# Performance work log

Measured on AMD Instinct MI355X. Metric: run time of the kernel, lower is better.

## Reference

```python
import jax, jax.numpy as jnp
import numpy as np

N = 50000
E = 800000
B = 64
NODE_IN, EDGE_IN, H, OUT_DIM = 16, 8, 64, 2


def _glorot(key, shape):
    fan_in, fan_out = shape[0], shape[-1]
    s = jnp.sqrt(6.0 / (fan_in + fan_out))
    return jax.random.uniform(key, shape, jnp.float32, -s, s)


def setup_inputs() -> dict:
    key = jax.random.key(0)
    ks = jax.random.split(key, 32)
    inp = {
        'x': jax.random.normal(ks[0], (N, NODE_IN), jnp.float32),
        'edge_index': jax.random.randint(ks[1], (2, E), 0, N).astype(jnp.int64),
        'edge_attr': jax.random.normal(ks[2], (E, EDGE_IN), jnp.float32),
        'batch': jnp.sort(jax.random.randint(ks[3], (N,), 0, B)).astype(jnp.int64),
        # encoders
        'W_node': _glorot(ks[4], (NODE_IN, H)), 'b_node': jnp.zeros((H,), jnp.float32),
        'W_edge': _glorot(ks[5], (EDGE_IN, H)), 'b_edge': jnp.zeros((H,), jnp.float32),
        # conv1: GATv2, heads=4, concat=True, edge_dim=H
        'Wl1': _glorot(ks[6], (H, 4 * H)), 'bl1': jnp.zeros((4 * H,), jnp.float32),
        'Wr1': _glorot(ks[7], (H, 4 * H)), 'br1': jnp.zeros((4 * H,), jnp.float32),
        'We1': _glorot(ks[8], (H, 4 * H)),
        'att1': _glorot(ks[9], (4, H)),
        'bias1': jnp.zeros((4 * H,), jnp.float32),
        # conv2: GATv2, heads=1, concat=False, in=4H
        'Wl2': _glorot(ks[10], (4 * H, H)), 'bl2': jnp.zeros((H,), jnp.float32),
        'Wr2': _glorot(ks[11], (4 * H, H)), 'br2': jnp.zeros((H,), jnp.float32),
        'We2': _glorot(ks[12], (H, H)),
        'att2': _glorot(ks[13], (1, H)),
        'bias2': jnp.zeros((H,), jnp.float32),
        # decoder
        'Wd1': _glorot(ks[14], (H, H)), 'bd1': jnp.zeros((H,), jnp.float32),
        'Wd2': _glorot(ks[15], (H, OUT_DIM)), 'bd2': jnp.zeros((OUT_DIM,), jnp.float32),
    }
    return inp


def _gatv2(x, src, dst, eattr, Wl, bl, Wr, br, We, att, bias, heads, out_ch, concat):
    n = x.shape[0]
    # add self-loops with edge_attr fill_value='mean' (segment mean over dst), PyG default
    ones = jnp.ones((src.shape[0],), x.dtype)
    deg = jax.ops.segment_sum(ones, dst, num_segments=n)
    loop_attr = jax.ops.segment_sum(eattr, dst, num_segments=n) / jnp.clip(deg, 1.0)[:, None]
    ea = jnp.concatenate([eattr, loop_attr], 0)               # [E+N, F_e]
    s = jnp.concatenate([src, jnp.arange(n)], 0)
    d = jnp.concatenate([dst, jnp.arange(n)], 0)
    xl = (x @ Wl + bl).reshape(n, heads, out_ch)              # source transform
    xr = (x @ Wr + br).reshape(n, heads, out_ch)              # target transform
    ep = (ea @ We).reshape(-1, heads, out_ch)                 # edge transform (no bias)
    m = jax.nn.leaky_relu(xl[s] + xr[d] + ep, 0.2)            # [E+N, heads, out_ch]
    logits = jnp.einsum('ehc,hc->eh', m, att)
    lmax = jax.ops.segment_max(logits, d, num_segments=n)
    lmax = jnp.where(jnp.isfinite(lmax), lmax, 0.0)
    a = jnp.exp(logits - lmax[d])
    denom = jax.ops.segment_sum(a, d, num_segments=n)
    alpha = a / (denom[d] + 1e-16)                            # segment softmax over dst
    out = jax.ops.segment_sum(alpha[..., None] * xl[s], d, num_segments=n)
    out = out.reshape(n, heads * out_ch) if concat else out.mean(1)
    return out + bias


def reference(x, edge_index, edge_attr, batch, W_node, b_node, W_edge, b_edge,
              Wl1, bl1, Wr1, br1, We1, att1, bias1,
              Wl2, bl2, Wr2, br2, We2, att2, bias2,
              Wd1, bd1, Wd2, bd2):
    src, dst = edge_index[0], edge_index[1]
    h = x @ W_node + b_node
    ea = edge_attr @ W_edge + b_edge
    h = jax.nn.elu(_gatv2(h, src, dst, ea, Wl1, bl1, Wr1, br1, We1, att1, bias1, 4, H, True))
    h = _gatv2(h, src, dst, ea, Wl2, bl2, Wr2, br2, We2, att2, bias2, 1, H, False)
    # global mean pool over batch vector
    cnt = jax.ops.segment_sum(jnp.ones((h.shape[0],), h.dtype), batch, num_segments=B)
    pooled = jax.ops.segment_sum(h, batch, num_segments=B) / jnp.clip(cnt, 1.0)[:, None]
    out = jax.nn.relu(pooled @ Wd1 + bd1) @ Wd2 + bd2
    return jax.nn.sigmoid(out)
```

## Files before the change

kernel.cpp:

```cpp
#include <hip/hip_runtime.h>
#include <math.h>

#define NN 50000
#define NE 800000
#define NB 64

__device__ __forceinline__ int permpos(int c) {
  return ((c & 63) << 2) | (((c >> 6) ^ c) & 3);
}

__global__ void k_zero(int* __restrict__ p, int n) {
  int i = blockIdx.x * blockDim.x + threadIdx.x;
  if (i < n) p[i] = 0;
}

__global__ void k_fuse(const float* __restrict__ Wn, const float* __restrict__ bn,
                       const float* __restrict__ We, const float* __restrict__ be,
                       const float* __restrict__ Wl1, const float* __restrict__ bl1,
                       const float* __restrict__ Wr1, const float* __restrict__ br1,
                       const float* __restrict__ We1, const float* __restrict__ We2,
                       const float* __restrict__ att1, const float* __restrict__ bias1,
                       float* __restrict__ wl1e, float* __restrict__ bl1e,
                       float* __restrict__ wr1e, float* __restrict__ br1e,
                       float* __restrict__ wfe1, float* __restrict__ bfe1,
                       float* __restrict__ wfe2, float* __restrict__ bfe2,
                       float* __restrict__ att1p, float* __restrict__ bias1p) {
  int t = blockIdx.x * blockDim.x + threadIdx.x;
  if (t < 4096) {
    int i = t >> 8, j = t & 255; float s = 0.f;
    for (int k = 0; k < 64; k++) s += Wn[i * 64 + k] * Wl1[k * 256 + j];
    wl1e[i * 256 + permpos(j)] = s;
  } else if (t < 8192) {
    int u = t - 4096; int i = u >> 8, j = u & 255; float s = 0.f;
    for (int k = 0; k < 64; k++) s += Wn[i * 64 + k] * Wr1[k * 256 + j];
    wr1e[i * 256 + permpos(j)] = s;
  } else if (t < 10240) {
    int u = t - 8192; int i = u >> 8, j = u & 255; float s = 0.f;
    for (int k = 0; k < 64; k++) s += We[i * 64 + k] * We1[k * 256 + j];
    wfe1[i * 256 + permpos(j)] = s;
  } else if (t < 10752) {
    int u = t - 10240; int i = u >> 6, j = u & 63; float s = 0.f;
    for (int k = 0; k < 64; k++) s += We[i * 64 + k] * We2[k * 64 + j];
    wfe2[u] = s;
  } else if (t < 11008) {
    int j = t - 10752; float s = bl1[j];
    for (int k = 0; k < 64; k++) s += bn[k] * Wl1[k * 256 + j];
    bl1e[permpos(j)] = s;
  } else if (t < 11264) {
    int j = t - 11008; float s = br1[j];
    for (int k = 0; k < 64; k++) s += bn[k] * Wr1[k * 256 + j];
    br1e[permpos(j)] = s;
  } else if (t < 11520) {
    int j = t - 11264; float s = 0.f;
    for (int k = 0; k < 64; k++) s += be[k] * We1[k * 256 + j];
    bfe1[permpos(j)] = s;
  } else if (t < 11584) {
    int j = t - 11520; float s = 0.f;
    for (int k = 0; k < 64; k++) s += be[k] * We2[k * 64 + j];
    bfe2[j] = s;
  } else if (t < 11840) {
    int j = t - 11584;
    att1p[permpos(j)] = att1[j];
  } else if (t < 12096) {
    int j = t - 11840;
    bias1p[permpos(j)] = bias1[j];
  }
}

__global__ void k_deg(const int* __restrict__ dstA, int* __restrict__ deg) {
  int e = blockIdx.x * blockDim.x + threadIdx.x;
  if (e < NE) atomicAdd(&deg[dstA[e]], 1);
}

__global__ __launch_bounds__(1024) void k_scan1(const int* __restrict__ deg,
                                                int* __restrict__ incl, int* __restrict__ partials) {
  __shared__ int sm[1024];
  int i = blockIdx.x * 1024 + threadIdx.x;
  int v = (i < NN) ? (deg[i] + 1) : 0;
  sm[threadIdx.x] = v;
  __syncthreads();
  for (int off = 1; off < 1024; off <<= 1) {
    int t = (threadIdx.x >= off) ? sm[threadIdx.x - off] : 0;
    __syncthreads();
    sm[threadIdx.x] += t;
    __syncthreads();
  }
  if (i < NN) incl[i] = sm[threadIdx.x];
  if (threadIdx.x == 1023) partials[blockIdx.x] = sm[1023];
}

__global__ void k_scan2(int* __restrict__ partials, int* __restrict__ rowptr, int nblk) {
  int t = threadIdx.x;
  int v = (t < nblk) ? partials[t] : 0;
  for (int off = 1; off < 64; off <<= 1) {
    int u = __shfl_up(v, off, 64);
    if (t >= off) v += u;
  }
  if (t < nblk) partials[t] = v;
  if (t == nblk - 1) rowptr[NN] = v;
}

__global__ void k_scan3(const int* __restrict__ deg, const int* __restrict__ incl,
                        const int* __restrict__ partials, int* __restrict__ rowptr) {
  int i = blockIdx.x * blockDim.x + threadIdx.x;
  if (i >= NN) return;
  int blk = i >> 10;
  int base = blk ? partials[blk - 1] : 0;
  rowptr[i] = base + incl[i] - (deg[i] + 1);
}

__global__ void k_csr(const int* __restrict__ srcA, const int* __restrict__ dstA,
                      const int* __restrict__ rowptr, const int* __restrict__ deg,
                      int* __restrict__ cursor, int2* __restrict__ csr) {
  int t = blockIdx.x * blockDim.x + threadIdx.x;
  if (t < NE) {
    int d = dstA[t];
    int pos = rowptr[d] + atomicAdd(&cursor[d], 1);
    csr[pos] = make_int2(t, srcA[t]);
  } else if (t < NE + NN) {
    int n = t - NE;
    csr[rowptr[n] + deg[n]] = make_int2(NE + n, n);
  }
}

__global__ __launch_bounds__(256) void k_loop8(const int* __restrict__ rowptr,
                                               const int2* __restrict__ csr,
                                               const float* __restrict__ eattr,
                                               float* __restrict__ lattr) {
  int d = (blockIdx.x * blockDim.x + threadIdx.x) >> 6;
  int lane = threadIdx.x & 63;
  if (d >= NN) return;
  int beg = rowptr[d], endReal = rowptr[d + 1] - 1;
  int k = lane & 7, sub = lane >> 3;
  float s = 0.f;
  for (int i = beg + sub; i < endReal; i += 8) {
    int eid = csr[i].x;
    s += eattr[(size_t)eid * 8 + k];
  }
  s += __shfl_xor(s, 8, 64);
  s += __shfl_xor(s, 16, 64);
  s += __shfl_xor(s, 32, 64);
  float invdeg = 1.f / fmaxf((float)(endReal - beg), 1.f);
  if (lane < 8) lattr[(size_t)d * 8 + lane] = s * invdeg;
}

__global__ __launch_bounds__(256) void k_lin1(const float* __restrict__ x,
                                              const float* __restrict__ wl, const float* __restrict__ bl,
                                              const float* __restrict__ wr, const float* __restrict__ br,
                                              float* __restrict__ xl, float* __restrict__ xr) {
  __shared__ float xs[4][16];
  int nb = blockIdx.x * 4;
  int t = threadIdx.x;
  if (t < 64) xs[t >> 4][t & 15] = x[nb * 16 + t];
  __syncthreads();
  float accl[4], accr[4];
  float blv = bl[t], brv = br[t];
#pragma unroll
  for (int u = 0; u < 4; u++) { accl[u] = blv; accr[u] = brv; }
#pragma unroll
  for (int k = 0; k < 16; k++) {
    float wlv = wl[k * 256 + t], wrv = wr[k * 256 + t];
#pragma unroll
    for (int u = 0; u < 4; u++) {
      accl[u] += xs[u][k] * wlv;
      accr[u] += xs[u][k] * wrv;
    }
  }
#pragma unroll
  for (int u = 0; u < 4; u++) {
    xl[(size_t)(nb + u) * 256 + t] = accl[u];
    xr[(size_t)(nb + u) * 256 + t] = accr[u];
  }
}

__device__ __forceinline__ void load_ek(const float* __restrict__ eattr,
                                        const float* __restrict__ lattr,
                                        int eid, float ek[8]) {
  const float* b; int ei;
  if (eid < NE) { b = eattr; ei = eid; } else { b = lattr; ei = eid - NE; }
  const float* p = b + (size_t)ei * 8;
#pragma unroll
  for (int k = 0; k < 8; k++) ek[k] = p[k];
}

__device__ __forceinline__ float jreduce(float part[4]) {
  part[0] += __shfl_xor(part[1], 1, 64);
  part[2] += __shfl_xor(part[3], 1, 64);
  float v = part[0] + __shfl_xor(part[2], 2, 64);
  v += __shfl_xor(v, 4, 64);
  v += __shfl_xor(v, 8, 64);
  v += __shfl_xor(v, 16, 64);
  v += __shfl_xor(v, 32, 64);
  return v;
}

__global__ __launch_bounds__(256) void k_conv1(
    const float* __restrict__ eattr, const float* __restrict__ lattr,
    const int* __restrict__ rowptr, const int2* __restrict__ csr,
    const float* __restrict__ xl, const float* __restrict__ xrg,
    const float* __restrict__ att1p, const float* __restrict__ bias1p,
    const float* __restrict__ wfe1, const float* __restrict__ bfe1,
    float* __restrict__ out1) {
  int d = __builtin_amdgcn_readfirstlane((blockIdx.x * blockDim.x + threadIdx.x) >> 6);
  int lane = threadIdx.x & 63;
  if (d >= NN) return;
  int l4 = lane << 2;
  float4 xr4 = *(const float4*)(xrg + (size_t)d * 256 + l4);
  float4 at4 = *(const float4*)(att1p + l4);
  float4 bf4 = *(const float4*)(bfe1 + l4);
  float4 wf[8];
#pragma unroll
  for (int k = 0; k < 8; k++) wf[k] = *(const float4*)(wfe1 + k * 256 + l4);

  float acc0 = 0.f, acc1 = 0.f, acc2 = 0.f, acc3 = 0.f;
  float mrun = -INFINITY, lrun = 0.f;
  int beg = rowptr[d], end = rowptr[d + 1];

  auto epart = [&](int eid, const float4& x4, float part[4]) {
    float ek[8];
    load_ek(eattr, lattr, eid, ek);
    float e0 = bf4.x, e1 = bf4.y, e2 = bf4.z, e3 = bf4.w;
#pragma unroll
    for (int k = 0; k < 8; k++) {
      e0 += ek[k] * wf[k].x;
      e1 += ek[k] * wf[k].y;
      e2 += ek[k] * wf[k].z;
      e3 += ek[k] * wf[k].w;
    }
    float m0 = x4.x + xr4.x + e0; m0 = (m0 > 0.f) ? m0 : 0.2f * m0;
    float m1 = x4.y + xr4.y + e1; m1 = (m1 > 0.f) ? m1 : 0.2f * m1;
    float m2 = x4.z + xr4.z + e2; m2 = (m2 > 0.f) ? m2 : 0.2f * m2;
    float m3 = x4.w + xr4.w + e3; m3 = (m3 > 0.f) ? m3 : 0.2f * m3;
    part[0] = at4.x * m0; part[1] = at4.y * m1;
    part[2] = at4.z * m2; part[3] = at4.w * m3;
  };

  int idx = beg;
  for (; idx + 4 <= end; idx += 4) {
    int2 e0 = csr[idx], e1 = csr[idx + 1], e2 = csr[idx + 2], e3 = csr[idx + 3];
    float4 x0 = *(const float4*)(xl + (size_t)e0.y * 256 + l4);
    float4 x1 = *(const float4*)(xl + (size_t)e1.y * 256 + l4);
    float4 x2 = *(const float4*)(xl + (size_t)e2.y * 256 + l4);
    float4 x3 = *(const float4*)(xl + (size_t)e3.y * 256 + l4);
    float pa[4], pb[4], pc[4], pd[4];
    epart(e0.x, x0, pa); epart(e1.x, x1, pb);
    epart(e2.x, x2, pc); epart(e3.x, x3, pd);
    float v0 = jreduce(pa), v1 = jreduce(pb), v2 = jreduce(pc), v3 = jreduce(pd);
    float gmax = fmaxf(fmaxf(v0, v1), fmaxf(v2, v3));
    if (__ballot(gmax > mrun)) {
      float nm = fmaxf(mrun, gmax);
      float sc = __expf(mrun - nm);
      mrun = nm; lrun *= sc;
      float sc1 = __shfl_xor(sc, 1, 64);
      float sc2 = __shfl_xor(sc, 2, 64);
      float sc3 = __shfl_xor(sc1, 2, 64);
      acc0 *= sc; acc1 *= sc1; acc2 *= sc2; acc3 *= sc3;
    }
    float q0 = __expf(v0 - mrun), q1 = __expf(v1 - mrun);
    float q2 = __expf(v2 - mrun), q3 = __expf(v3 - mrun);
    lrun += q0 + q1 + q2 + q3;
    {
      float a1 = __shfl_xor(q0, 1, 64), a2 = __shfl_xor(q0, 2, 64), a3 = __shfl_xor(a1, 2, 64);
      acc0 += q0 * x0.x; acc1 += a1 * x0.y; acc2 += a2 * x0.z; acc3 += a3 * x0.w;
    }
    {
      float a1 = __shfl_xor(q1, 1, 64), a2 = __shfl_xor(q1, 2, 64), a3 = __shfl_xor(a1, 2, 64);
      acc0 += q1 * x1.x; acc1 += a1 * x1.y; acc2 += a2 * x1.z; acc3 += a3 * x1.w;
    }
    {
      float a1 = __shfl_xor(q2, 1, 64), a2 = __shfl_xor(q2, 2, 64), a3 = __shfl_xor(a1, 2, 64);
      acc0 += q2 * x2.x; acc1 += a1 * x2.y; acc2 += a2 * x2.z; acc3 += a3 * x2.w;
    }
    {
      float a1 = __shfl_xor(q3, 1, 64), a2 = __shfl_xor(q3, 2, 64), a3 = __shfl_xor(a1, 2, 64);
      acc0 += q3 * x3.x; acc1 += a1 * x3.y; acc2 += a2 * x3.z; acc3 += a3 * x3.w;
    }
  }
  for (; idx < end; ++idx) {
    int2 e0 = csr[idx];
    float4 x0 = *(const float4*)(xl + (size_t)e0.y * 256 + l4);
    float pa[4];
    epart(e0.x, x0, pa);
    float v0 = jreduce(pa);
    if (__ballot(v0 > mrun)) {
      float nm = fmaxf(mrun, v0);
      float sc = __expf(mrun - nm);
      mrun = nm; lrun *= sc;
      float sc1 = __shfl_xor(sc, 1, 64);
      float sc2 = __shfl_xor(sc, 2, 64);
      float sc3 = __shfl_xor(sc1, 2, 64);
      acc0 *= sc; acc1 *= sc1; acc2 *= sc2; acc3 *= sc3;
    }
    float q0 = __expf(v0 - mrun);
    lrun += q0;
    float a1 = __shfl_xor(q0, 1, 64), a2 = __shfl_xor(q0, 2, 64), a3 = __shfl_xor(a1, 2, 64);
    acc0 += q0 * x0.x; acc1 += a1 * x0.y; acc2 += a2 * x0.z; acc3 += a3 * x0.w;
  }

  float lr0 = lrun;
  float lr1 = __shfl_xor(lr0, 1, 64);
  float lr2 = __shfl_xor(lr0, 2, 64);
  float lr3 = __shfl_xor(lr1, 2, 64);
  float4 bi4 = *(const float4*)(bias1p + l4);
  float4 o;
  o.x = acc0 / (lr0 + 1e-16f) + bi4.x;
  o.y = acc1 / (lr1 + 1e-16f) + bi4.y;
  o.z = acc2 / (lr2 + 1e-16f) + bi4.z;
  o.w = acc3 / (lr3 + 1e-16f) + bi4.w;
  o.x = (o.x > 0.f) ? o.x : (__expf(o.x) - 1.f);
  o.y = (o.y > 0.f) ? o.y : (__expf(o.y) - 1.f);
  o.z = (o.z > 0.f) ? o.z : (__expf(o.z) - 1.f);
  o.w = (o.w > 0.f) ? o.w : (__expf(o.w) - 1.f);
  *(float4*)(out1 + (size_t)d * 256 + l4) = o;
}

__global__ __launch_bounds__(256) void k_lin2(const float* __restrict__ in,
                                              const float* __restrict__ wl, const float* __restrict__ bl,
                                              const float* __restrict__ wr, const float* __restrict__ br,
                                              float* __restrict__ xl, float* __restrict__ xr) {
  int col = threadIdx.x & 63;
  int grp = threadIdx.x >> 6;
  int node0 = blockIdx.x * 16 + grp * 4;
  float sl[4], sr[4];
  float blv = bl[col], brv = br[col];
#pragma unroll
  for (int u = 0; u < 4; u++) { sl[u] = blv; sr[u] = brv; }
  const float4* r0 = (const float4*)(in + (size_t)(node0 + 0) * 256);
  const float4* r1 = (const float4*)(in + (size_t)(node0 + 1) * 256);
  const float4* r2 = (const float4*)(in + (size_t)(node0 + 2) * 256);
  const float4* r3 = (const float4*)(in + (size_t)(node0 + 3) * 256);
#pragma unroll 4
  for (int g4 = 0; g4 < 64; g4++) {
    int b = g4 & 3;
    int i0 = ((0 ^ b) << 6) + g4;
    int i1 = ((1 ^ b) << 6) + g4;
    int i2 = ((2 ^ b) << 6) + g4;
    int i3 = ((3 ^ b) << 6) + g4;
    float wl0 = wl[i0 * 64 + col], wl1v = wl[i1 * 64 + col];
    float wl2v = wl[i2 * 64 + col], wl3v = wl[i3 * 64 + col];
    float wr0 = wr[i0 * 64 + col], wr1v = wr[i1 * 64 + col];
    float wr2v = wr[i2 * 64 + col], wr3v = wr[i3 * 64 + col];
    float4 v0 = r0[g4], v1 = r1[g4], v2 = r2[g4], v3 = r3[g4];
    sl[0] += v0.x * wl0 + v0.y * wl1v + v0.z * wl2v + v0.w * wl3v;
    sl[1] += v1.x * wl0 + v1.y * wl1v + v1.z * wl2v + v1.w * wl3v;
    sl[2] += v2.x * wl0 + v2.y * wl1v + v2.z * wl2v + v2.w * wl3v;
    sl[3] += v3.x * wl0 + v3.y * wl1v + v3.z * wl2v + v3.w * wl3v;
    sr[0] += v0.x * wr0 + v0.y * wr1v + v0.z * wr2v + v0.w * wr3v;
    sr[1] += v1.x * wr0 + v1.y * wr1v + v1.z * wr2v + v1.w * wr3v;
    sr[2] += v2.x * wr0 + v2.y * wr1v + v2.z * wr2v + v2.w * wr3v;
    sr[3] += v3.x * wr0 + v3.y * wr1v + v3.z * wr2v + v3.w * wr3v;
  }
#pragma unroll
  for (int u = 0; u < 4; u++) {
    xl[(size_t)(node0 + u) * 64 + col] = sl[u];
    xr[(size_t)(node0 + u) * 64 + col] = sr[u];
  }
}

__global__ __launch_bounds__(256) void k_conv2(
    const float* __restrict__ eattr, const float* __restrict__ lattr,
    const int* __restrict__ rowptr, const int2* __restrict__ csr,
    const float* __restrict__ xl, const float* __restrict__ xrg,
    const float* __restrict__ att2, const float* __restrict__ bias2,
    const float* __restrict__ wfe2, const float* __restrict__ bfe2,
    float* __restrict__ out2) {
  int d = __builtin_amdgcn_readfirstlane((blockIdx.x * blockDim.x + threadIdx.x) >> 6);
  int lane = threadIdx.x & 63;
  if (d >= NN) return;
  float xr_l = xrg[(size_t)d * 64 + lane];
  float att_l = att2[lane];
  float bfe_l = bfe2[lane];
  float wfe_l[8];
#pragma unroll
  for (int k = 0; k < 8; k++) wfe_l[k] = wfe2[k * 64 + lane];
  float acc = 0.f, mrun = -INFINITY, lrun = 0.f;
  int beg = rowptr[d], end = rowptr[d + 1];

  auto elogit = [&](int eid, float xs) {
    float ek[8];
    load_ek(eattr, lattr, eid, ek);
    float ep = bfe_l;
#pragma unroll
    for (int k = 0; k < 8; k++) ep += ek[k] * wfe_l[k];
    float m = xs + xr_l + ep;
    m = (m > 0.f) ? m : 0.2f * m;
    float v = att_l * m;
    v += __shfl_xor(v, 1, 64);
    v += __shfl_xor(v, 2, 64);
    v += __shfl_xor(v, 4, 64);
    v += __shfl_xor(v, 8, 64);
    v += __shfl_xor(v, 16, 64);
    v += __shfl_xor(v, 32, 64);
    return v;
  };

  int idx = beg;
  for (; idx + 4 <= end; idx += 4) {
    int2 e0 = csr[idx], e1 = csr[idx + 1], e2 = csr[idx + 2], e3 = csr[idx + 3];
    float x0 = xl[(size_t)e0.y * 64 + lane];
    float x1 = xl[(size_t)e1.y * 64 + lane];
    float x2 = xl[(size_t)e2.y * 64 + lane];
    float x3 = xl[(size_t)e3.y * 64 + lane];
    float v0 = elogit(e0.x, x0), v1 = elogit(e1.x, x1);
    float v2 = elogit(e2.x, x2), v3 = elogit(e3.x, x3);
    float gmax = fmaxf(fmaxf(v0, v1), fmaxf(v2, v3));
    if (gmax > mrun) {
      float sc = __expf(mrun - gmax);
      mrun = gmax; lrun *= sc; acc *= sc;
    }
    float q0 = __expf(v0 - mrun), q1 = __expf(v1 - mrun);
    float q2 = __expf(v2 - mrun), q3 = __expf(v3 - mrun);
    lrun += q0 + q1 + q2 + q3;
    acc += q0 * x0 + q1 * x1 + q2 * x2 + q3 * x3;
  }
  for (; idx < end; ++idx) {
    int2 e0 = csr[idx];
    float x0 = xl[(size_t)e0.y * 64 + lane];
    float v0 = elogit(e0.x, x0);
    if (v0 > mrun) {
      float sc = __expf(mrun - v0);
      mrun = v0; lrun *= sc; acc *= sc;
    }
    float q0 = __expf(v0 - mrun);
    lrun += q0;
    acc += q0 * x0;
  }
  out2[(size_t)d * 64 + lane] = acc / (lrun + 1e-16f) + bias2[lane];
}

__device__ __forceinline__ int lowerb(const int* a, int n, int v) {
  int lo = 0, hi = n;
  while (lo < hi) {
    int mid = (lo + hi) >> 1;
    if (a[mid] < v) lo = mid + 1; else hi = mid;
  }
  return lo;
}

__global__ __launch_bounds__(256) void k_pool(const int* __restrict__ batch,
                                              const float* __restrict__ out2,
                                              float* __restrict__ pooled) {
  int b = blockIdx.x;
  int start = lowerb(batch, NN, b);
  int end = lowerb(batch, NN, b + 1);
  int c = threadIdx.x & 63, sub = threadIdx.x >> 6;
  float s = 0.f;
  for (int i = start + sub; i < end; i += 4) s += out2[(size_t)i * 64 + c];
  __shared__ float sm[256];
  sm[threadIdx.x] = s;
  __syncthreads();
  if (sub == 0) {
    float tot = sm[c] + sm[64 + c] + sm[128 + c] + sm[192 + c];
    float cnt = fmaxf((float)(end - start), 1.f);
    pooled[b * 64 + c] = tot / cnt;
  }
}

__global__ __launch_bounds__(1024) void k_dec(const float* __restrict__ pooled,
                                              const float* __restrict__ Wd1, const float* __restrict__ bd1,
                                              const float* __restrict__ Wd2, const float* __restrict__ bd2,
                                              float* __restrict__ out) {
  __shared__ float hid[64 * 64];
  int t = threadIdx.x;
  for (int i = t; i < 4096; i += 1024) {
    int b = i >> 6, j = i & 63;
    float s = bd1[j];
#pragma unroll 8
    for (int k = 0; k < 64; k++) s += pooled[b * 64 + k] * Wd1[k * 64 + j];
    hid[i] = fmaxf(s, 0.f);
  }
  __syncthreads();
  if (t < 128) {
    int b = t >> 1, o = t & 1;
    float s = bd2[o];
#pragma unroll 8
    for (int k = 0; k < 64; k++) s += hid[b * 64 + k] * Wd2[k * 2 + o];
    out[t] = 1.f / (1.f + __expf(-s));
  }
}

extern "C" void kernel_launch(void* const* d_in, const int* in_sizes, int n_in,
                              void* d_out, int out_size, void* d_ws, size_t ws_size,
                              hipStream_t stream) {
  const float* x     = (const float*)d_in[0];
  const int*   eidx  = (const int*)d_in[1];
  const float* eattr = (const float*)d_in[2];
  const int*   batch = (const int*)d_in[3];
  const float* Wn    = (const float*)d_in[4];
  const float* bn    = (const float*)d_in[5];
  const float* We    = (const float*)d_in[6];
  const float* be    = (const float*)d_in[7];
  const float* Wl1   = (const float*)d_in[8];
  const float* bl1   = (const float*)d_in[9];
  const float* Wr1   = (const float*)d_in[10];
  const float* br1   = (const float*)d_in[11];
  const float* We1   = (const float*)d_in[12];
  const float* att1  = (const float*)d_in[13];
  const float* bias1 = (const float*)d_in[14];
  const float* Wl2   = (const float*)d_in[15];
  const float* bl2   = (const float*)d_in[16];
  const float* Wr2   = (const float*)d_in[17];
  const float* br2   = (const float*)d_in[18];
  const float* We2   = (const float*)d_in[19];
  const float* att2  = (const float*)d_in[20];
  const float* bias2 = (const float*)d_in[21];
  const float* Wd1   = (const float*)d_in[22];
  const float* bd1   = (const float*)d_in[23];
  const float* Wd2   = (const float*)d_in[24];
  const float* bd2   = (const float*)d_in[25];

  const int* srcA = eidx;
  const int* dstA = eidx + NE;

  char* ws = (char*)d_ws;
  size_t off = 0;
  auto alloc = [&](size_t bytes) -> char* {
    char* p = ws + off;
    off += (bytes + 255) & ~(size_t)255;
    return p;
  };

  int*   deg    = (int*)alloc(NN * 4);
  int*   cursor = (int*)alloc(NN * 4);
  size_t zero_bytes = off;
  int*   rowptr   = (int*)alloc((NN + 1) * 4);
  int*   incl     = (int*)alloc(NN * 4);
  int*   partials = (int*)alloc(64 * 4);
  int2*  csr      = (int2*)alloc((size_t)(NE + NN + 1) * 8);
  float* lattr = (float*)alloc((size_t)NN * 8 * 4);
  float* wl1e  = (float*)alloc(4096 * 4);
  float* wr1e  = (float*)alloc(4096 * 4);
  float* wfe1  = (float*)alloc(2048 * 4);
  float* wfe2  = (float*)alloc(512 * 4);
  float* bl1e  = (float*)alloc(256 * 4);
  float* br1e  = (float*)alloc(256 * 4);
  float* bfe1  = (float*)alloc(256 * 4);
  float* bfe2  = (float*)alloc(64 * 4);
  float* att1p = (float*)alloc(256 * 4);
  float* bias1p= (float*)alloc(256 * 4);
  float* xl1   = (float*)alloc((size_t)NN * 256 * 4);
  float* xr1   = (float*)alloc((size_t)NN * 256 * 4);
  float* out1  = (float*)alloc((size_t)NN * 256 * 4);
  float* xl2   = (float*)alloc((size_t)NN * 64 * 4);
  float* xr2   = (float*)alloc((size_t)NN * 64 * 4);
  float* out2  = (float*)alloc((size_t)NN * 64 * 4);
  float* pooled = (float*)alloc((size_t)NB * 64 * 4);

  int zn = (int)(zero_bytes / 4);
  int nscan = (NN + 1023) / 1024;
  k_zero<<<(zn + 255) / 256, 256, 0, stream>>>((int*)d_ws, zn);
  k_fuse<<<(12096 + 255) / 256, 256, 0, stream>>>(Wn, bn, We, be, Wl1, bl1, Wr1, br1, We1, We2,
                                                  att1, bias1,
                                                  wl1e, bl1e, wr1e, br1e, wfe1, bfe1, wfe2, bfe2,
                                                  att1p, bias1p);
  k_deg<<<(NE + 255) / 256, 256, 0, stream>>>(dstA, deg);
  k_scan1<<<nscan, 1024, 0, stream>>>(deg, incl, partials);
  k_scan2<<<1, 64, 0, stream>>>(partials, rowptr, nscan);
  k_scan3<<<(NN + 255) / 256, 256, 0, stream>>>(deg, incl, partials, rowptr);
  k_csr<<<(NE + NN + 255) / 256, 256, 0, stream>>>(srcA, dstA, rowptr, deg, cursor, csr);
  k_loop8<<<(NN + 3) / 4, 256, 0, stream>>>(rowptr, csr, eattr, lattr);
  k_lin1<<<NN / 4, 256, 0, stream>>>(x, wl1e, bl1e, wr1e, br1e, xl1, xr1);
  k_conv1<<<(NN + 3) / 4, 256, 0, stream>>>(eattr, lattr, rowptr, csr, xl1, xr1,
                                            att1p, bias1p, wfe1, bfe1, out1);
  k_lin2<<<NN / 16, 256, 0, stream>>>(out1, Wl2, bl2, Wr2, br2, xl2, xr2);
  k_conv2<<<(NN + 3) / 4, 256, 0, stream>>>(eattr, lattr, rowptr, csr, xl2, xr2,
                                            att2, bias2, wfe2, bfe2, out2);
  k_pool<<<NB, 256, 0, stream>>>(batch, out2, pooled);
  k_dec<<<1, 1024, 0, stream>>>(pooled, Wd1, bd1, Wd2, bd2, (float*)d_out);
}
```

Measured before the change: 771.4 us.

## Store gathered source features as bf16 and restructure conv/lin reductions

```diff
diff --git a/kernel.cpp b/kernel.cpp
--- a/kernel.cpp
+++ b/kernel.cpp
@@ -7,6 +7,15 @@
 
 __device__ __forceinline__ int permpos(int c) {
   return ((c & 63) << 2) | (((c >> 6) ^ c) & 3);
+}
+
+__device__ __forceinline__ unsigned short f2bf(float f) {
+  unsigned int u = __float_as_uint(f);
+  u += 0x7fffu + ((u >> 16) & 1u);
+  return (unsigned short)(u >> 16);
+}
+__device__ __forceinline__ float bf2f(unsigned short b) {
+  return __uint_as_float(((unsigned int)b) << 16);
 }
 
 __global__ void k_zero(int* __restrict__ p, int n) {
@@ -147,40 +156,34 @@
 __global__ __launch_bounds__(256) void k_lin1(const float* __restrict__ x,
                                               const float* __restrict__ wl, const float* __restrict__ bl,
                                               const float* __restrict__ wr, const float* __restrict__ br,
-                                              float* __restrict__ xl, float* __restrict__ xr) {
+                                              unsigned short* __restrict__ xl, float* __restrict__ xr) {
   __shared__ float xs[4][16];
   int nb = blockIdx.x * 4;
   int t = threadIdx.x;
   if (t < 64) xs[t >> 4][t & 15] = x[nb * 16 + t];
   __syncthreads();
-  float accl[4], accr[4];
-  float blv = bl[t], brv = br[t];
-#pragma unroll
-  for (int u = 0; u < 4; u++) { accl[u] = blv; accr[u] = brv; }
+  int w = t >> 6, lane = t & 63, l4 = lane << 2;
+  float4 accl = *(const float4*)(bl + l4);
+  float4 accr = *(const float4*)(br + l4);
+  const float* xrow = xs[w];
 #pragma unroll
   for (int k = 0; k < 16; k++) {
-    float wlv = wl[k * 256 + t], wrv = wr[k * 256 + t];
-#pragma unroll
-    for (int u = 0; u < 4; u++) {
-      accl[u] += xs[u][k] * wlv;
-      accr[u] += xs[u][k] * wrv;
-    }
-  }
-#pragma unroll
-  for (int u = 0; u < 4; u++) {
-    xl[(size_t)(nb + u) * 256 + t] = accl[u];
-    xr[(size_t)(nb + u) * 256 + t] = accr[u];
-  }
-}
-
-__device__ __forceinline__ void load_ek(const float* __restrict__ eattr,
-                                        const float* __restrict__ lattr,
-                                        int eid, float ek[8]) {
-  const float* b; int ei;
-  if (eid < NE) { b = eattr; ei = eid; } else { b = lattr; ei = eid - NE; }
-  const float* p = b + (size_t)ei * 8;
-#pragma unroll
-  for (int k = 0; k < 8; k++) ek[k] = p[k];
+    float xv = xrow[k];
+    float4 wl4 = *(const float4*)(wl + k * 256 + l4);
+    float4 wr4 = *(const float4*)(wr + k * 256 + l4);
+    accl.x += xv * wl4.x; accl.y += xv * wl4.y; accl.z += xv * wl4.z; accl.w += xv * wl4.w;
+    accr.x += xv * wr4.x; accr.y += xv * wr4.y; accr.z += xv * wr4.z; accr.w += xv * wr4.w;
+  }
+  int node = nb + w;
+  ushort4 us;
+  us.x = f2bf(accl.x); us.y = f2bf(accl.y); us.z = f2bf(accl.z); us.w = f2bf(accl.w);
+  *(ushort4*)(xl + (size_t)node * 256 + l4) = us;
+  *(float4*)(xr + (size_t)node * 256 + l4) = accr;
+}
+
+__device__ __forceinline__ const float* ek_ptr(const float* __restrict__ eattr,
+                                               const float* __restrict__ lattr, int eid) {
+  return (eid < NE) ? (eattr + (size_t)eid * 8) : (lattr + (size_t)(eid - NE) * 8);
 }
 
 __device__ __forceinline__ float jreduce(float part[4]) {
@@ -197,7 +200,7 @@
 __global__ __launch_bounds__(256) void k_conv1(
     const float* __restrict__ eattr, const float* __restrict__ lattr,
     const int* __restrict__ rowptr, const int2* __restrict__ csr,
-    const float* __restrict__ xl, const float* __restrict__ xrg,
+    const unsigned short* __restrict__ xl, const float* __restrict__ xrg,
     const float* __restrict__ att1p, const float* __restrict__ bias1p,
     const float* __restrict__ wfe1, const float* __restrict__ bfe1,
     float* __restrict__ out1) {
@@ -216,16 +219,18 @@
   float mrun = -INFINITY, lrun = 0.f;
   int beg = rowptr[d], end = rowptr[d + 1];
 
-  auto epart = [&](int eid, const float4& x4, float part[4]) {
-    float ek[8];
-    load_ek(eattr, lattr, eid, ek);
+  auto ld4 = [&](int s) -> float4 {
+    ushort4 u = *(const ushort4*)(xl + (size_t)s * 256 + l4);
+    float4 f; f.x = bf2f(u.x); f.y = bf2f(u.y); f.z = bf2f(u.z); f.w = bf2f(u.w);
+    return f;
+  };
+  auto epart = [&](const float* __restrict__ p, const float4& x4, float part[4]) {
     float e0 = bf4.x, e1 = bf4.y, e2 = bf4.z, e3 = bf4.w;
 #pragma unroll
     for (int k = 0; k < 8; k++) {
-      e0 += ek[k] * wf[k].x;
-      e1 += ek[k] * wf[k].y;
-      e2 += ek[k] * wf[k].z;
-      e3 += ek[k] * wf[k].w;
+      float ekv = p[k];
+      e0 += ekv * wf[k].x; e1 += ekv * wf[k].y;
+      e2 += ekv * wf[k].z; e3 += ekv * wf[k].w;
     }
     float m0 = x4.x + xr4.x + e0; m0 = (m0 > 0.f) ? m0 : 0.2f * m0;
     float m1 = x4.y + xr4.y + e1; m1 = (m1 > 0.f) ? m1 : 0.2f * m1;
@@ -238,13 +243,16 @@
   int idx = beg;
   for (; idx + 4 <= end; idx += 4) {
     int2 e0 = csr[idx], e1 = csr[idx + 1], e2 = csr[idx + 2], e3 = csr[idx + 3];
-    float4 x0 = *(const float4*)(xl + (size_t)e0.y * 256 + l4);
-    float4 x1 = *(const float4*)(xl + (size_t)e1.y * 256 + l4);
-    float4 x2 = *(const float4*)(xl + (size_t)e2.y * 256 + l4);
-    float4 x3 = *(const float4*)(xl + (size_t)e3.y * 256 + l4);
+    int s0 = __builtin_amdgcn_readfirstlane(e0.y), id0 = __builtin_amdgcn_readfirstlane(e0.x);
+    int s1 = __builtin_amdgcn_readfirstlane(e1.y), id1 = __builtin_amdgcn_readfirstlane(e1.x);
+    int s2 = __builtin_amdgcn_readfirstlane(e2.y), id2 = __builtin_amdgcn_readfirstlane(e2.x);
+    int s3 = __builtin_amdgcn_readfirstlane(e3.y), id3 = __builtin_amdgcn_readfirstlane(e3.x);
+    float4 x0 = ld4(s0), x1 = ld4(s1), x2 = ld4(s2), x3 = ld4(s3);
     float pa[4], pb[4], pc[4], pd[4];
-    epart(e0.x, x0, pa); epart(e1.x, x1, pb);
-    epart(e2.x, x2, pc); epart(e3.x, x3, pd);
+    epart(ek_ptr(eattr, lattr, id0), x0, pa);
+    epart(ek_ptr(eattr, lattr, id1), x1, pb);
+    epart(ek_ptr(eattr, lattr, id2), x2, pc);
+    epart(ek_ptr(eattr, lattr, id3), x3, pd);
     float v0 = jreduce(pa), v1 = jreduce(pb), v2 = jreduce(pc), v3 = jreduce(pd);
     float gmax = fmaxf(fmaxf(v0, v1), fmaxf(v2, v3));
     if (__ballot(gmax > mrun)) {
@@ -278,9 +286,10 @@
   }
   for (; idx < end; ++idx) {
     int2 e0 = csr[idx];
-    float4 x0 = *(const float4*)(xl + (size_t)e0.y * 256 + l4);
+    int s0 = __builtin_amdgcn_readfirstlane(e0.y), id0 = __builtin_amdgcn_readfirstlane(e0.x);
+    float4 x0 = ld4(s0);
     float pa[4];
-    epart(e0.x, x0, pa);
+    epart(ek_ptr(eattr, lattr, id0), x0, pa);
     float v0 = jreduce(pa);
     if (__ballot(v0 > mrun)) {
       float nm = fmaxf(mrun, v0);
@@ -317,19 +326,18 @@
 __global__ __launch_bounds__(256) void k_lin2(const float* __restrict__ in,
                                               const float* __restrict__ wl, const float* __restrict__ bl,
                                               const float* __restrict__ wr, const float* __restrict__ br,
-                                              float* __restrict__ xl, float* __restrict__ xr) {
+                                              unsigned short* __restrict__ xl, float* __restrict__ xr) {
   int col = threadIdx.x & 63;
   int grp = threadIdx.x >> 6;
-  int node0 = blockIdx.x * 16 + grp * 4;
-  float sl[4], sr[4];
+  int node0 = blockIdx.x * 32 + grp * 8;
+  float sl[8], sr[8];
   float blv = bl[col], brv = br[col];
 #pragma unroll
-  for (int u = 0; u < 4; u++) { sl[u] = blv; sr[u] = brv; }
-  const float4* r0 = (const float4*)(in + (size_t)(node0 + 0) * 256);
-  const float4* r1 = (const float4*)(in + (size_t)(node0 + 1) * 256);
-  const float4* r2 = (const float4*)(in + (size_t)(node0 + 2) * 256);
-  const float4* r3 = (const float4*)(in + (size_t)(node0 + 3) * 256);
-#pragma unroll 4
+  for (int u = 0; u < 8; u++) { sl[u] = blv; sr[u] = brv; }
+  const float4* r[8];
+#pragma unroll
+  for (int u = 0; u < 8; u++) r[u] = (const float4*)(in + (size_t)(node0 + u) * 256);
+#pragma unroll 2
   for (int g4 = 0; g4 < 64; g4++) {
     int b = g4 & 3;
     int i0 = ((0 ^ b) << 6) + g4;
@@ -340,27 +348,27 @@
     float wl2v = wl[i2 * 64 + col], wl3v = wl[i3 * 64 + col];
     float wr0 = wr[i0 * 64 + col], wr1v = wr[i1 * 64 + col];
     float wr2v = wr[i2 * 64 + col], wr3v = wr[i3 * 64 + col];
-    float4 v0 = r0[g4], v1 = r1[g4], v2 = r2[g4], v3 = r3[g4];
-    sl[0] += v0.x * wl0 + v0.y * wl1v + v0.z * wl2v + v0.w * wl3v;
-    sl[1] += v1.x * wl0 + v1.y * wl1v + v1.z * wl2v + v1.w * wl3v;
-    sl[2] += v2.x * wl0 + v2.y * wl1v + v2.z * wl2v + v2.w * wl3v;
-    sl[3] += v3.x * wl0 + v3.y * wl1v + v3.z * wl2v + v3.w * wl3v;
-    sr[0] += v0.x * wr0 + v0.y * wr1v + v0.z * wr2v + v0.w * wr3v;
-    sr[1] += v1.x * wr0 + v1.y * wr1v + v1.z * wr2v + v1.w * wr3v;
-    sr[2] += v2.x * wr0 + v2.y * wr1v + v2.z * wr2v + v2.w * wr3v;
-    sr[3] += v3.x * wr0 + v3.y * wr1v + v3.z * wr2v + v3.w * wr3v;
-  }
-#pragma unroll
-  for (int u = 0; u < 4; u++) {
-    xl[(size_t)(node0 + u) * 64 + col] = sl[u];
-    xr[(size_t)(node0 + u) * 64 + col] = sr[u];
+#pragma unroll
+    for (int u = 0; u < 8; u++) {
+      float4 v = r[u][g4];
+      sl[u] += v.x * wl0 + v.y * wl1v + v.z * wl2v + v.w * wl3v;
+      sr[u] += v.x * wr0 + v.y * wr1v + v.z * wr2v + v.w * wr3v;
+    }
+  }
+#pragma unroll
+  for (int u = 0; u < 8; u++) {
+    int node = node0 + u;
+    if (node < NN) {
+      xl[(size_t)node * 64 + col] = f2bf(sl[u]);
+      xr[(size_t)node * 64 + col] = sr[u];
+    }
   }
 }
 
 __global__ __launch_bounds__(256) void k_conv2(
     const float* __restrict__ eattr, const float* __restrict__ lattr,
     const int* __restrict__ rowptr, const int2* __restrict__ csr,
-    const float* __restrict__ xl, const float* __restrict__ xrg,
+    const unsigned short* __restrict__ xl, const float* __restrict__ xrg,
     const float* __restrict__ att2, const float* __restrict__ bias2,
     const float* __restrict__ wfe2, const float* __restrict__ bfe2,
     float* __restrict__ out2) {
@@ -375,55 +383,79 @@
   for (int k = 0; k < 8; k++) wfe_l[k] = wfe2[k * 64 + lane];
   float acc = 0.f, mrun = -INFINITY, lrun = 0.f;
   int beg = rowptr[d], end = rowptr[d + 1];
-
-  auto elogit = [&](int eid, float xs) {
-    float ek[8];
-    load_ek(eattr, lattr, eid, ek);
+  bool b0 = (lane & 1), b1 = (lane & 2);
+
+  auto pl = [&](const float* __restrict__ p, float xs) {
     float ep = bfe_l;
 #pragma unroll
-    for (int k = 0; k < 8; k++) ep += ek[k] * wfe_l[k];
+    for (int k = 0; k < 8; k++) ep += p[k] * wfe_l[k];
     float m = xs + xr_l + ep;
     m = (m > 0.f) ? m : 0.2f * m;
-    float v = att_l * m;
+    return att_l * m;
+  };
+
+  int idx = beg;
+  for (; idx + 4 <= end; idx += 4) {
+    int2 e0 = csr[idx], e1 = csr[idx + 1], e2 = csr[idx + 2], e3 = csr[idx + 3];
+    int s0 = __builtin_amdgcn_readfirstlane(e0.y), id0 = __builtin_amdgcn_readfirstlane(e0.x);
+    int s1 = __builtin_amdgcn_readfirstlane(e1.y), id1 = __builtin_amdgcn_readfirstlane(e1.x);
+    int s2 = __builtin_amdgcn_readfirstlane(e2.y), id2 = __builtin_amdgcn_readfirstlane(e2.x);
+    int s3 = __builtin_amdgcn_readfirstlane(e3.y), id3 = __builtin_amdgcn_readfirstlane(e3.x);
+    float x0 = bf2f(xl[(size_t)s0 * 64 + lane]);
+    float x1 = bf2f(xl[(size_t)s1 * 64 + lane]);
+    float x2 = bf2f(xl[(size_t)s2 * 64 + lane]);
+    float x3 = bf2f(xl[(size_t)s3 * 64 + lane]);
+    float v0 = pl(ek_ptr(eattr, lattr, id0), x0);
+    float v1 = pl(ek_ptr(eattr, lattr, id1), x1);
+    float v2 = pl(ek_ptr(eattr, lattr, id2), x2);
+    float v3 = pl(ek_ptr(eattr, lattr, id3), x3);
+    float a01 = b0 ? v1 : v0;
+    a01 += __shfl_xor(b0 ? v0 : v1, 1, 64);
+    float a23 = b0 ? v3 : v2;
+    a23 += __shfl_xor(b0 ? v2 : v3, 1, 64);
+    float w = b1 ? a23 : a01;
+    w += __shfl_xor(b1 ? a01 : a23, 2, 64);
+    w += __shfl_xor(w, 4, 64);
+    w += __shfl_xor(w, 8, 64);
+    w += __shfl_xor(w, 16, 64);
+    w += __shfl_xor(w, 32, 64);
+    float g = fmaxf(w, __shfl_xor(w, 1, 64));
+    g = fmaxf(g, __shfl_xor(g, 2, 64));
+    if (g > mrun) {
+      float sc = __expf(mrun - g);
+      mrun = g; lrun *= sc; acc *= sc;
+    }
+    float q = __expf(w - mrun);
+    float q1 = __shfl_xor(q, 1, 64);
+    float q2 = __shfl_xor(q, 2, 64);
+    float q3 = __shfl_xor(q1, 2, 64);
+    lrun += (q + q1) + (q2 + q3);
+    float u01 = b0 ? x1 : x0, u10 = b0 ? x0 : x1;
+    float u23 = b0 ? x3 : x2, u32 = b0 ? x2 : x3;
+    float xr0 = b1 ? u23 : u01;
+    float xr1v = b1 ? u32 : u10;
+    float xr2v = b1 ? u01 : u23;
+    float xr3v = b1 ? u10 : u32;
+    acc += q * xr0 + q1 * xr1v + q2 * xr2v + q3 * xr3v;
+  }
+  for (; idx < end; ++idx) {
+    int2 e0 = csr[idx];
+    int s0 = __builtin_amdgcn_readfirstlane(e0.y), id0 = __builtin_amdgcn_readfirstlane(e0.x);
+    float x0 = bf2f(xl[(size_t)s0 * 64 + lane]);
+    float v = pl(ek_ptr(eattr, lattr, id0), x0);
     v += __shfl_xor(v, 1, 64);
     v += __shfl_xor(v, 2, 64);
     v += __shfl_xor(v, 4, 64);
     v += __shfl_xor(v, 8, 64);
     v += __shfl_xor(v, 16, 64);
     v += __shfl_xor(v, 32, 64);
-    return v;
-  };
-
-  int idx = beg;
-  for (; idx + 4 <= end; idx += 4) {
-    int2 e0 = csr[idx], e1 = csr[idx + 1], e2 = csr[idx + 2], e3 = csr[idx + 3];
-    float x0 = xl[(size_t)e0.y * 64 + lane];
-    float x1 = xl[(size_t)e1.y * 64 + lane];
-    float x2 = xl[(size_t)e2.y * 64 + lane];
-    float x3 = xl[(size_t)e3.y * 64 + lane];
-    float v0 = elogit(e0.x, x0), v1 = elogit(e1.x, x1);
-    float v2 = elogit(e2.x, x2), v3 = elogit(e3.x, x3);
-    float gmax = fmaxf(fmaxf(v0, v1), fmaxf(v2, v3));
-    if (gmax > mrun) {
-      float sc = __expf(mrun - gmax);
-      mrun = gmax; lrun *= sc; acc *= sc;
-    }
-    float q0 = __expf(v0 - mrun), q1 = __expf(v1 - mrun);
-    float q2 = __expf(v2 - mrun), q3 = __expf(v3 - mrun);
-    lrun += q0 + q1 + q2 + q3;
-    acc += q0 * x0 + q1 * x1 + q2 * x2 + q3 * x3;
-  }
-  for (; idx < end; ++idx) {
-    int2 e0 = csr[idx];
-    float x0 = xl[(size_t)e0.y * 64 + lane];
-    float v0 = elogit(e0.x, x0);
-    if (v0 > mrun) {
-      float sc = __expf(mrun - v0);
-      mrun = v0; lrun *= sc; acc *= sc;
-    }
-    float q0 = __expf(v0 - mrun);
-    lrun += q0;
-    acc += q0 * x0;
+    if (v > mrun) {
+      float sc = __expf(mrun - v);
+      mrun = v; lrun *= sc; acc *= sc;
+    }
+    float q = __expf(v - mrun);
+    lrun += q;
+    acc += q * x0;
   }
   out2[(size_t)d * 64 + lane] = acc / (lrun + 1e-16f) + bias2[lane];
 }
@@ -538,10 +570,10 @@
   float* bfe2  = (float*)alloc(64 * 4);
   float* att1p = (float*)alloc(256 * 4);
   float* bias1p= (float*)alloc(256 * 4);
-  float* xl1   = (float*)alloc((size_t)NN * 256 * 4);
+  unsigned short* xl1 = (unsigned short*)alloc((size_t)NN * 256 * 2);
   float* xr1   = (float*)alloc((size_t)NN * 256 * 4);
   float* out1  = (float*)alloc((size_t)NN * 256 * 4);
-  float* xl2   = (float*)alloc((size_t)NN * 64 * 4);
+  unsigned short* xl2 = (unsigned short*)alloc((size_t)NN * 64 * 2);
   float* xr2   = (float*)alloc((size_t)NN * 64 * 4);
   float* out2  = (float*)alloc((size_t)NN * 64 * 4);
   float* pooled = (float*)alloc((size_t)NB * 64 * 4);
@@ -562,7 +594,7 @@
   k_lin1<<<NN / 4, 256, 0, stream>>>(x, wl1e, bl1e, wr1e, br1e, xl1, xr1);
   k_conv1<<<(NN + 3) / 4, 256, 0, stream>>>(eattr, lattr, rowptr, csr, xl1, xr1,
                                             att1p, bias1p, wfe1, bfe1, out1);
-  k_lin2<<<NN / 16, 256, 0, stream>>>(out1, Wl2, bl2, Wr2, br2, xl2, xr2);
+  k_lin2<<<(NN + 31) / 32, 256, 0, stream>>>(out1, Wl2, bl2, Wr2, br2, xl2, xr2);
   k_conv2<<<(NN + 3) / 4, 256, 0, stream>>>(eattr, lattr, rowptr, csr, xl2, xr2,
                                             att2, bias2, wfe2, bfe2, out2);
   k_pool<<<NB, 256, 0, stream>>>(batch, out2, pooled);
```

Measured after the change: 771.7 us. No clear change (+0.0%).
